# Performance work log

Measured on AMD Instinct MI355X. Metric: run time of the kernel, lower is better.

The kernel has to match this reference:

```python
import jax, jax.numpy as jnp
import numpy as np

F_DIM = 128
EC = 32
SYM = 16
B = 4
S = 2048
EPS = 1e-5


def rpy_to_rot(a):
    # roll-pitch-yaw euler angles [..., 3] -> rotation matrices [..., 3, 3]
    c, s = jnp.cos(a), jnp.sin(a)
    cr, cp, cy = c[..., 0], c[..., 1], c[..., 2]
    sr, sp, sy = s[..., 0], s[..., 1], s[..., 2]
    return jnp.stack([
        jnp.stack([cy * cp, cy * sp * sr - sy * cr, cy * sp * cr + sy * sr], -1),
        jnp.stack([sy * cp, sy * sp * sr + cy * cr, sy * sp * cr - cy * sr], -1),
        jnp.stack([-sp, cp * sr, cp * cr], -1),
    ], -2)


def _tile(x):
    # tile_for_symgroups: append the first SYM (symmetric) elements again
    return jnp.concatenate([x, x[:, :SYM]], axis=1)


def _cbn(emb, h, bw, bb, gw, gb):
    # BatchedCBatchNormLayer in eval mode: running_mean=0, running_var=1 buffers
    beta = emb @ bw + bb
    gamma = emb @ gw + gb
    hn = h * (1.0 / np.sqrt(1.0 + EPS))
    return gamma[:, None, :] * hn + beta[:, None, :]


def _forward(packed_vector, samples, fc1_w, fc1_b, bn1_beta_w, bn1_beta_b, bn1_gamma_w, bn1_gamma_b, rfc1_w, rfc1_b, bn2_beta_w, bn2_beta_b, bn2_gamma_w, bn2_gamma_b, rfc2_w, rfc2_b, bn3_beta_w, bn3_beta_b, bn3_gamma_w, bn3_gamma_b, fc2_w, fc2_b):
    b = packed_vector.shape[0]
    constants = packed_vector[..., 0:1]
    centers = packed_vector[..., 1:4]
    radii = packed_vector[..., 4:10]   # 3 stds + 3 euler angles
    iparams = packed_vector[..., 10:]

    eff_const = _tile(constants)       # [B, E, 1]
    eff_centers = _tile(centers)       # [B, E, 3]
    eff_radii = _tile(radii)           # [B, E, 6]
    eff_iparams = _tile(iparams)       # [B, E, F]
    e = EC + SYM

    samp = jnp.broadcast_to(samples[:, None], (b, EC, samples.shape[1], 3))
    sym_samp = samp[:, :SYM] * jnp.array([1.0, 1.0, -1.0], samples.dtype)  # left-right reflection
    eff_samples = jnp.concatenate([samp, sym_samp], axis=1)                # [B, E, S, 3]

    # quadric algebraic distance (quadric has only the constant term at [3, 3])
    quad = jnp.zeros((b, e, 4, 4), samples.dtype).at[..., 3, 3].set(eff_const[..., 0])
    diff = eff_samples - eff_centers[:, :, None, :]
    homog = jnp.concatenate([diff, jnp.ones(diff.shape[:-1] + (1,), diff.dtype)], -1)
    half = jnp.einsum('besj,beij->besi', homog, quad)
    per_element_constants = jnp.sum(half * homog, -1, keepdims=True)       # [B, E, S, 1]

    # gaussian RBF influence weights in the rotated element frame
    rot = rpy_to_rot(eff_radii[..., 3:6])                                  # [B, E, 3, 3]
    local_diff = jnp.einsum('besi,beij->besj', diff, rot)                  # R^T (x - c)
    std = jnp.maximum(eff_radii[..., :3], 1e-4)
    local_samples = local_diff / std[:, :, None, :]                        # world2local = S(1/std) R^T T(-c)
    per_element_weights = jnp.exp(-0.5 * jnp.sum(local_samples ** 2, -1, keepdims=True))

    # OccNet decoder over flattened batch*element
    emb = eff_iparams.reshape(b * e, F_DIM)
    x = local_samples.reshape(b * e, -1, 3)
    h = x @ fc1_w + fc1_b                                                  # [BE, S, F]
    h = _cbn(emb, h, bn1_beta_w, bn1_beta_b, bn1_gamma_w, bn1_gamma_b)
    init_h = h
    h = jax.nn.relu(h) @ rfc1_w + rfc1_b
    h = _cbn(emb, h, bn2_beta_w, bn2_beta_b, bn2_gamma_w, bn2_gamma_b)
    h = jax.nn.relu(h) @ rfc2_w + rfc2_b
    h = init_h + h
    h = _cbn(emb, h, bn3_beta_w, bn3_beta_b, bn3_gamma_w, bn3_gamma_b)
    vals = h @ fc2_w + fc2_b                                               # [BE, S, 1]

    implicit_values = vals.reshape(b, e, -1, 1)
    residuals = 1.0 + implicit_values
    local_decisions = per_element_constants * per_element_weights * residuals
    sdf = jnp.sum(local_decisions, axis=1)                                 # [B, S, 1]
    return sdf


def setup_inputs():
    key = jax.random.key(0)
    ks = jax.random.split(key, 16)
    const = jax.random.normal(ks[0], (B, EC, 1), dtype=jnp.float32) * 0.5
    centers = jax.random.normal(ks[1], (B, EC, 3), dtype=jnp.float32) * 0.5
    radii_std = jax.random.uniform(ks[2], (B, EC, 3), dtype=jnp.float32, minval=0.1, maxval=0.4)
    euler = jax.random.uniform(ks[3], (B, EC, 3), dtype=jnp.float32, minval=-np.pi, maxval=np.pi)
    iparams = jax.random.normal(ks[4], (B, EC, F_DIM), dtype=jnp.float32)
    packed_vector = jnp.concatenate([const, centers, radii_std, euler, iparams], -1)
    samples = jax.random.normal(ks[5], (B, S, 3), dtype=jnp.float32)

    def lin(k, i, o):
        kw, kb = jax.random.split(k)
        return (jax.random.normal(kw, (i, o), dtype=jnp.float32) / np.sqrt(i),
                jax.random.normal(kb, (o,), dtype=jnp.float32) * 0.01)

    fc1_w, fc1_b = lin(ks[6], 3, F_DIM)
    bn1_beta_w, bn1_beta_b = lin(ks[7], F_DIM, F_DIM)
    bn1_gamma_w, bn1_gamma_b = lin(ks[8], F_DIM, F_DIM)
    rfc1_w, rfc1_b = lin(ks[9], F_DIM, F_DIM)
    bn2_beta_w, bn2_beta_b = lin(ks[10], F_DIM, F_DIM)
    bn2_gamma_w, bn2_gamma_b = lin(ks[11], F_DIM, F_DIM)
    rfc2_w, rfc2_b = lin(ks[12], F_DIM, F_DIM)
    bn3_beta_w, bn3_beta_b = lin(ks[13], F_DIM, F_DIM)
    bn3_gamma_w, bn3_gamma_b = lin(ks[14], F_DIM, F_DIM)
    fc2_w, fc2_b = lin(ks[15], F_DIM, 1)
    return {"packed_vector": packed_vector, "samples": samples,
            "fc1_w": fc1_w, "fc1_b": fc1_b,
            "bn1_beta_w": bn1_beta_w, "bn1_beta_b": bn1_beta_b,
            "bn1_gamma_w": bn1_gamma_w, "bn1_gamma_b": bn1_gamma_b,
            "rfc1_w": rfc1_w, "rfc1_b": rfc1_b,
            "bn2_beta_w": bn2_beta_w, "bn2_beta_b": bn2_beta_b,
            "bn2_gamma_w": bn2_gamma_w, "bn2_gamma_b": bn2_gamma_b,
            "rfc2_w": rfc2_w, "rfc2_b": rfc2_b,
            "bn3_beta_w": bn3_beta_w, "bn3_beta_b": bn3_beta_b,
            "bn3_gamma_w": bn3_gamma_w, "bn3_gamma_b": bn3_gamma_b,
            "fc2_w": fc2_w, "fc2_b": fc2_b}


def reference(packed_vector, samples, fc1_w, fc1_b, bn1_beta_w, bn1_beta_b, bn1_gamma_w, bn1_gamma_b, rfc1_w, rfc1_b, bn2_beta_w, bn2_beta_b, bn2_gamma_w, bn2_gamma_b, rfc2_w, rfc2_b, bn3_beta_w, bn3_beta_b, bn3_gamma_w, bn3_gamma_b, fc2_w, fc2_b):
    return _forward(packed_vector, samples, fc1_w, fc1_b, bn1_beta_w, bn1_beta_b, bn1_gamma_w, bn1_gamma_b, rfc1_w, rfc1_b, bn2_beta_w, bn2_beta_b, bn2_gamma_w, bn2_gamma_b, rfc2_w, rfc2_b, bn3_beta_w, bn3_beta_b, bn3_gamma_w, bn3_gamma_b, fc2_w, fc2_b)
```

## Files before the change

### kernel.cpp

```cpp
#include <hip/hip_runtime.h>
#include <math.h>

#define B_   4
#define EC_  32
#define E_   48
#define S_   2048
#define F_   128

typedef __attribute__((ext_vector_type(8)))  short short8;
typedef __attribute__((ext_vector_type(4)))  float f32x4;
typedef __attribute__((ext_vector_type(16))) float f32x16;

__device__ __align__(16) short g_A1[4 * 8 * 64 * 8];

#define PKF2 1440
__device__ __align__(16) float g_bepark[B_ * E_ * PKF2];

static __device__ __forceinline__ short f2bf(float x) {
    unsigned u = __float_as_uint(x);
    unsigned r = (u + 0x7FFFu + ((u >> 16) & 1u)) >> 16;
    return (short)r;
}

__global__ __launch_bounds__(256) void precompute_kernel(
    const float* __restrict__ packed,
    const float* __restrict__ fc1w, const float* __restrict__ fc1b,
    const float* __restrict__ bw1, const float* __restrict__ bb1,
    const float* __restrict__ gw1, const float* __restrict__ gb1,
    const float* __restrict__ rb1g, const float* __restrict__ rw1,
    const float* __restrict__ bw2, const float* __restrict__ bb2,
    const float* __restrict__ gw2, const float* __restrict__ gb2,
    const float* __restrict__ rw2, const float* __restrict__ rb2g,
    const float* __restrict__ bw3, const float* __restrict__ bb3,
    const float* __restrict__ gw3, const float* __restrict__ gb3,
    const float* __restrict__ fc2w, const float* __restrict__ fc2b)
{
    const int be = blockIdx.x;

    if (be >= 192) {
        const int unit = (be - 192) * 4 + (threadIdx.x >> 6);
        const int l  = threadIdx.x & 63;
        const int MT = unit >> 3;
        const int ks = unit & 7;
        const int fo = MT * 32 + (l & 31);
        const int q1 = l >> 5;
        short8 v;
        #pragma unroll
        for (int j = 0; j < 8; ++j) {
            const int fi = (ks >> 1) * 32 + (ks & 1) * 16 + ((j >> 2) & 1) * 8 +
                           (j & 3) + q1 * 4;
            v[j] = f2bf(rw1[fi * F_ + fo]);
        }
        *(short8*)&g_A1[((MT * 8 + ks) * 64 + l) * 8] = v;
        return;
    }

    const int b  = be / E_;
    const int e  = be - b * E_;
    const int ec = (e < EC_) ? e : (e - EC_);
    const float* pv = packed + (size_t)(b * EC_ + ec) * 138;
    float* P = g_bepark + (size_t)be * PKF2;

    __shared__ float emb[F_];
    __shared__ float part[6][2][F_];
    __shared__ float g3s[F_];
    __shared__ float redbuf[F_];

    const int t = threadIdx.x & 127;
    const int h = threadIdx.x >> 7;
    if (h == 0) emb[t] = pv[10 + t];
    __syncthreads();

    float a0 = 0.f, a1 = 0.f, a2 = 0.f, a3 = 0.f, a4 = 0.f, a5 = 0.f;
    for (int k = h * 64; k < h * 64 + 64; ++k) {
        const float ek = emb[k];
        a0 = fmaf(ek, bw1[k * F_ + t], a0);
        a1 = fmaf(ek, gw1[k * F_ + t], a1);
        a2 = fmaf(ek, bw2[k * F_ + t], a2);
        a3 = fmaf(ek, gw2[k * F_ + t], a3);
        a4 = fmaf(ek, bw3[k * F_ + t], a4);
        a5 = fmaf(ek, gw3[k * F_ + t], a5);
    }
    part[0][h][t] = a0; part[1][h][t] = a1; part[2][h][t] = a2;
    part[3][h][t] = a3; part[4][h][t] = a4; part[5][h][t] = a5;
    __syncthreads();

    const float inv = 0.99999500003749984f;
    if (h == 0) {
        const float sb1 = part[0][0][t] + part[0][1][t];
        const float sg1 = part[1][0][t] + part[1][1][t];
        const float sb2 = part[2][0][t] + part[2][1][t];
        const float sg2 = part[3][0][t] + part[3][1][t];
        const float sb3 = part[4][0][t] + part[4][1][t];
        const float sg3 = part[5][0][t] + part[5][1][t];

        const float g1p = (sg1 + gb1[t]) * inv;
        const float b1  =  sb1 + bb1[t];
        const float g2p = (sg2 + gb2[t]) * inv;
        const float b2p = fmaf(g2p, rb1g[t], sb2 + bb2[t]);
        const float g3  = (sg3 + gb3[t]) * inv * fc2w[t];

        P[0 * F_ + t] = g2p;
        P[1 * F_ + t] = b2p;
        g3s[t] = g3;
        redbuf[t] = (sb3 + bb3[t]) * fc2w[t] + g3 * rb2g[t];

        const float w0p = g1p * fc1w[t];
        const float w1p = g1p * fc1w[F_ + t];
        const float w2p = g1p * fc1w[2 * F_ + t];
        const float pbp = fmaf(g1p, fc1b[t], b1);
        short* A0 = (short*)(P + 416);
        const int MTl = t >> 5, fl = t & 31;
        short8 v  = {f2bf(w0p), f2bf(w1p), f2bf(w2p), f2bf(pbp), 0, 0, 0, 0};
        short8 zz = {0, 0, 0, 0, 0, 0, 0, 0};
        *(short8*)&A0[(MTl * 64 + fl) * 8]      = v;
        *(short8*)&A0[(MTl * 64 + 32 + fl) * 8] = zz;

        part[1][0][t] = g3 * w0p;
        part[2][0][t] = g3 * w1p;
        part[3][0][t] = g3 * w2p;
        part[4][0][t] = g3 * pbp;
    }
    __syncthreads();

    {
        float ua = 0.f;
        const float* wrow = rw2 + (size_t)t * F_ + h * 64;
        #pragma unroll
        for (int f4 = 0; f4 < 64; f4 += 4) {
            const f32x4 wv = *(const f32x4*)&wrow[f4];
            const int fb = h * 64 + f4;
            ua = fmaf(wv[0], g3s[fb + 0], ua);
            ua = fmaf(wv[1], g3s[fb + 1], ua);
            ua = fmaf(wv[2], g3s[fb + 2], ua);
            ua = fmaf(wv[3], g3s[fb + 3], ua);
        }
        part[0][h][t] = ua;
    }
    __syncthreads();
    if (h == 0) P[2 * F_ + t] = part[0][0][t] + part[0][1][t];

    if (threadIdx.x == 0) {
        float cb = fc2b[0];
        float w30 = 0.f, w31 = 0.f, w32 = 0.f, w3b = 0.f;
        for (int i = 0; i < F_; ++i) {
            cb  += redbuf[i];
            w30 += part[1][0][i];
            w31 += part[2][0][i];
            w32 += part[3][0][i];
            w3b += part[4][0][i];
        }
        P[400] = w30; P[401] = w31; P[402] = w32; P[403] = w3b + cb;

        const float sx = fmaxf(pv[4], 1e-4f);
        const float sy = fmaxf(pv[5], 1e-4f);
        const float sz = fmaxf(pv[6], 1e-4f);
        const float ar = pv[7], ap = pv[8], ay = pv[9];
        const float cr = cosf(ar), sr = sinf(ar);
        const float cp = cosf(ap), sp = sinf(ap);
        const float cyw = cosf(ay), syw = sinf(ay);
        float* g = P + 384;
        g[0] = pv[0]; g[1] = pv[1]; g[2] = pv[2]; g[3] = pv[3];
        g[4] = 1.f / sx; g[5] = 1.f / sy; g[6] = 1.f / sz;
        g[7]  = cyw * cp;  g[8]  = cyw * sp * sr - syw * cr;  g[9]  = cyw * sp * cr + syw * sr;
        g[10] = syw * cp;  g[11] = syw * sp * sr + cyw * cr;  g[12] = syw * sp * cr - cyw * sr;
        g[13] = -sp;       g[14] = cp * sr;                   g[15] = cp * cr;
    }
}

__global__ __launch_bounds__(256, 2) void ldif_main(
    const float* __restrict__ samples, float* __restrict__ out)
{
    const int bid = blockIdx.x;
    const int eg  = bid & 7;
    const int seg = (bid >> 3) & 15;
    const int b   = bid >> 7;
    const int be0 = b * E_ + eg * 6;

    __shared__ __align__(16) short lsA1[4 * 8 * 64 * 8];
    __shared__ __align__(16) float lsPar[6 * 416];

    const int tid = threadIdx.x;

    {
        const f32x4* src = (const f32x4*)g_A1;
        f32x4* dst = (f32x4*)lsA1;
        #pragma unroll
        for (int i = 0; i < 8; ++i) dst[i * 256 + tid] = src[i * 256 + tid];
    }
    for (int i = tid; i < 624; i += 256) {
        const int ei = i / 104;
        const int o4 = i - ei * 104;
        ((f32x4*)lsPar)[ei * 104 + o4] =
            *(const f32x4*)&g_bepark[(size_t)(be0 + ei) * PKF2 + o4 * 4];
    }
    __syncthreads();

    const int l   = tid & 63;
    const int w   = tid >> 6;
    const int q1  = l >> 5;
    const int l31 = l & 31;
    const int sidx = seg * 128 + w * 32 + l31;
    const f32x16 z16 = {0.f,0.f,0.f,0.f,0.f,0.f,0.f,0.f,
                        0.f,0.f,0.f,0.f,0.f,0.f,0.f,0.f};

    const float* sp = samples + ((size_t)b * S_ + sidx) * 3;
    const float xs = sp[0], ys = sp[1], zs0 = sp[2];

    float acc = 0.f;

    #pragma unroll
    for (int ee = 0; ee < 6; ++ee) {
        const int pe = ee * 416;
        const float* gg = &lsPar[pe + 384];
        const float* w3 = &lsPar[pe + 400];
        const int e = eg * 6 + ee;

        float cwgt, sval;
        union { short8 s8; unsigned u[4]; } b0u;
        b0u.u[0] = 0; b0u.u[1] = 0; b0u.u[2] = 0; b0u.u[3] = 0;
        {
            const float zz = (e >= EC_) ? -zs0 : zs0;
            const float dx = xs - gg[1], dy = ys - gg[2], dz = zz - gg[3];
            const float l0 = (dx * gg[7] + dy * gg[10] + dz * gg[13]) * gg[4];
            const float l1 = (dx * gg[8] + dy * gg[11] + dz * gg[14]) * gg[5];
            const float l2 = (dx * gg[9] + dy * gg[12] + dz * gg[15]) * gg[6];
            cwgt = gg[0] * __expf(-0.5f * (l0 * l0 + l1 * l1 + l2 * l2));
            sval = fmaf(l0, w3[0], fmaf(l1, w3[1], fmaf(l2, w3[2], w3[3])));
            if (q1 == 0) {
                const float one = 1.0f;
                unsigned p01, p23;
                asm("v_cvt_pk_bf16_f32 %0, %1, %2" : "=v"(p01) : "v"(l0), "v"(l1));
                asm("v_cvt_pk_bf16_f32 %0, %1, %2" : "=v"(p23) : "v"(l2), "v"(one));
                b0u.u[0] = p01; b0u.u[1] = p23;
            }
        }
        const short8 b0 = b0u.s8;

        const short* A0g = (const short*)(g_bepark + (size_t)(be0 + ee) * PKF2 + 416);
        f32x16 d0[4];
        #pragma unroll
        for (int MT = 0; MT < 4; ++MT) {
            const short8 a0 = *(const short8*)&A0g[(MT * 64 + l) * 8];
            d0[MT] = __builtin_amdgcn_mfma_f32_32x32x16_bf16(a0, b0, z16, 0, 0, 0);
        }

        f32x16 d1[4];
        #pragma unroll
        for (int MT = 0; MT < 4; ++MT) d1[MT] = z16;
        #pragma unroll
        for (int ks = 0; ks < 8; ++ks) {
            union { short8 s8; unsigned u[4]; } b1u;
            #pragma unroll
            for (int jj = 0; jj < 4; ++jj) {
                const int j0 = jj * 2;
                const int r0 = (j0 & 3) + 4 * ((j0 >> 2) & 1) + 8 * (ks & 1);
                const float v0 = fmaxf(d0[ks >> 1][r0], 0.f);
                const float v1 = fmaxf(d0[ks >> 1][r0 + 1], 0.f);
                asm("v_cvt_pk_bf16_f32 %0, %1, %2" : "=v"(b1u.u[jj]) : "v"(v0), "v"(v1));
            }
            const short8 b1 = b1u.s8;
            #pragma unroll
            for (int MT = 0; MT < 4; ++MT) {
                const short8 a = *(const short8*)&lsA1[((MT * 8 + ks) * 64 + l) * 8];
                d1[MT] = __builtin_amdgcn_mfma_f32_32x32x16_bf16(a, b1, d1[MT], 0, 0, 0);
            }
        }

        float part = 0.f;
        #pragma unroll
        for (int MT = 0; MT < 4; ++MT) {
            #pragma unroll
            for (int c = 0; c < 4; ++c) {
                const int fb = MT * 32 + c * 8 + q1 * 4;
                const f32x4 g2 = *(const f32x4*)&lsPar[pe + fb];
                const f32x4 b2 = *(const f32x4*)&lsPar[pe + 128 + fb];
                const f32x4 uu = *(const f32x4*)&lsPar[pe + 256 + fb];
                #pragma unroll
                for (int i = 0; i < 4; ++i) {
                    const float tt = fmaf(g2[i], d1[MT][c * 4 + i], b2[i]);
                    part = fmaf(fmaxf(tt, 0.f), uu[i], part);
                }
            }
        }
        part += __shfl_xor(part, 32);
        acc = fmaf(cwgt, 1.f + part + sval, acc);
    }

    if (l < 32) atomicAdd(&out[(size_t)b * S_ + sidx], acc);
}

extern "C" void kernel_launch(void* const* d_in, const int* in_sizes, int n_in,
                              void* d_out, int out_size, void* d_ws, size_t ws_size,
                              hipStream_t stream) {
    (void)in_sizes; (void)n_in; (void)d_ws; (void)ws_size;

    const float* packed  = (const float*)d_in[0];
    const float* samples = (const float*)d_in[1];
    const float* fc1w = (const float*)d_in[2];
    const float* fc1b = (const float*)d_in[3];
    const float* bw1  = (const float*)d_in[4];
    const float* bb1  = (const float*)d_in[5];
    const float* gw1  = (const float*)d_in[6];
    const float* gb1  = (const float*)d_in[7];
    const float* rw1  = (const float*)d_in[8];
    const float* rb1  = (const float*)d_in[9];
    const float* bw2  = (const float*)d_in[10];
    const float* bb2  = (const float*)d_in[11];
    const float* gw2  = (const float*)d_in[12];
    const float* gb2  = (const float*)d_in[13];
    const float* rw2  = (const float*)d_in[14];
    const float* rb2  = (const float*)d_in[15];
    const float* bw3  = (const float*)d_in[16];
    const float* bb3  = (const float*)d_in[17];
    const float* gw3  = (const float*)d_in[18];
    const float* gb3  = (const float*)d_in[19];
    const float* fc2w = (const float*)d_in[20];
    const float* fc2b = (const float*)d_in[21];
    float* out = (float*)d_out;

    (void)hipMemsetAsync(out, 0, (size_t)out_size * sizeof(float), stream);

    precompute_kernel<<<200, 256, 0, stream>>>(
        packed, fc1w, fc1b,
        bw1, bb1, gw1, gb1, rb1, rw1,
        bw2, bb2, gw2, gb2, rw2, rb2,
        bw3, bb3, gw3, gb3, fc2w, fc2b);

    ldif_main<<<512, 256, 0, stream>>>(samples, out);
}
```

Before: 39.30 us.

## Replace memset and atomics with workspace partials plus reduce kernel; widen precompute blocks

The main kernel now writes per-element-group partial sums into a workspace instead of atomically adding into a zeroed output. A small reduce kernel sums the 8 partials, which removes both the memset launch and the atomic contention. The precompute kernel also moves to 512 threads per block, splitting its K loops four ways to shorten each thread's serial dot products. The cost is an extra kernel launch and workspace traffic in place of the memset launch.

```diff
diff --git a/kernel.cpp b/kernel.cpp
--- a/kernel.cpp
+++ b/kernel.cpp
@@ -22,7 +22,7 @@
     return (short)r;
 }
 
-__global__ __launch_bounds__(256) void precompute_kernel(
+__global__ __launch_bounds__(512) void precompute_kernel(
     const float* __restrict__ packed,
     const float* __restrict__ fc1w, const float* __restrict__ fc1b,
     const float* __restrict__ bw1, const float* __restrict__ bb1,
@@ -38,7 +38,7 @@
     const int be = blockIdx.x;
 
     if (be >= 192) {
-        const int unit = (be - 192) * 4 + (threadIdx.x >> 6);
+        const int unit = (be - 192) * 8 + (threadIdx.x >> 6);
         const int l  = threadIdx.x & 63;
         const int MT = unit >> 3;
         const int ks = unit & 7;
@@ -62,7 +62,7 @@
     float* P = g_bepark + (size_t)be * PKF2;
 
     __shared__ float emb[F_];
-    __shared__ float part[6][2][F_];
+    __shared__ float part[6][4][F_];
     __shared__ float g3s[F_];
     __shared__ float redbuf[F_];
 
@@ -72,7 +72,7 @@
     __syncthreads();
 
     float a0 = 0.f, a1 = 0.f, a2 = 0.f, a3 = 0.f, a4 = 0.f, a5 = 0.f;
-    for (int k = h * 64; k < h * 64 + 64; ++k) {
+    for (int k = h * 32; k < h * 32 + 32; ++k) {
         const float ek = emb[k];
         a0 = fmaf(ek, bw1[k * F_ + t], a0);
         a1 = fmaf(ek, gw1[k * F_ + t], a1);
@@ -87,12 +87,12 @@
 
     const float inv = 0.99999500003749984f;
     if (h == 0) {
-        const float sb1 = part[0][0][t] + part[0][1][t];
-        const float sg1 = part[1][0][t] + part[1][1][t];
-        const float sb2 = part[2][0][t] + part[2][1][t];
-        const float sg2 = part[3][0][t] + part[3][1][t];
-        const float sb3 = part[4][0][t] + part[4][1][t];
-        const float sg3 = part[5][0][t] + part[5][1][t];
+        const float sb1 = part[0][0][t] + part[0][1][t] + part[0][2][t] + part[0][3][t];
+        const float sg1 = part[1][0][t] + part[1][1][t] + part[1][2][t] + part[1][3][t];
+        const float sb2 = part[2][0][t] + part[2][1][t] + part[2][2][t] + part[2][3][t];
+        const float sg2 = part[3][0][t] + part[3][1][t] + part[3][2][t] + part[3][3][t];
+        const float sb3 = part[4][0][t] + part[4][1][t] + part[4][2][t] + part[4][3][t];
+        const float sg3 = part[5][0][t] + part[5][1][t] + part[5][2][t] + part[5][3][t];
 
         const float g1p = (sg1 + gb1[t]) * inv;
         const float b1  =  sb1 + bb1[t];
@@ -125,20 +125,21 @@
 
     {
         float ua = 0.f;
-        const float* wrow = rw2 + (size_t)t * F_ + h * 64;
-        #pragma unroll
-        for (int f4 = 0; f4 < 64; f4 += 4) {
+        const float* wrow = rw2 + (size_t)t * F_ + h * 32;
+        #pragma unroll
+        for (int f4 = 0; f4 < 32; f4 += 4) {
             const f32x4 wv = *(const f32x4*)&wrow[f4];
-            const int fb = h * 64 + f4;
+            const int fb = h * 32 + f4;
             ua = fmaf(wv[0], g3s[fb + 0], ua);
             ua = fmaf(wv[1], g3s[fb + 1], ua);
             ua = fmaf(wv[2], g3s[fb + 2], ua);
             ua = fmaf(wv[3], g3s[fb + 3], ua);
         }
-        part[0][h][t] = ua;
-    }
-    __syncthreads();
-    if (h == 0) P[2 * F_ + t] = part[0][0][t] + part[0][1][t];
+        part[5][h][t] = ua;
+    }
+    __syncthreads();
+    if (h == 0)
+        P[2 * F_ + t] = part[5][0][t] + part[5][1][t] + part[5][2][t] + part[5][3][t];
 
     if (threadIdx.x == 0) {
         float cb = fc2b[0];
@@ -169,7 +170,7 @@
 }
 
 __global__ __launch_bounds__(256, 2) void ldif_main(
-    const float* __restrict__ samples, float* __restrict__ out)
+    const float* __restrict__ samples, float* __restrict__ ws)
 {
     const int bid = blockIdx.x;
     const int eg  = bid & 7;
@@ -287,13 +288,25 @@
         acc = fmaf(cwgt, 1.f + part + sval, acc);
     }
 
-    if (l < 32) atomicAdd(&out[(size_t)b * S_ + sidx], acc);
+    if (l < 32)
+        ws[(size_t)eg * (B_ * S_) + (size_t)b * S_ + sidx] = acc;
+}
+
+__global__ __launch_bounds__(256) void reduce_kernel(
+    const float* __restrict__ ws, float* __restrict__ out)
+{
+    const int i = blockIdx.x * 256 + threadIdx.x;
+    float s = 0.f;
+    #pragma unroll
+    for (int eg = 0; eg < 8; ++eg)
+        s += ws[(size_t)eg * (B_ * S_) + i];
+    out[i] = s;
 }
 
 extern "C" void kernel_launch(void* const* d_in, const int* in_sizes, int n_in,
                               void* d_out, int out_size, void* d_ws, size_t ws_size,
                               hipStream_t stream) {
-    (void)in_sizes; (void)n_in; (void)d_ws; (void)ws_size;
+    (void)in_sizes; (void)n_in; (void)out_size; (void)ws_size;
 
     const float* packed  = (const float*)d_in[0];
     const float* samples = (const float*)d_in[1];
@@ -318,14 +331,15 @@
     const float* fc2w = (const float*)d_in[20];
     const float* fc2b = (const float*)d_in[21];
     float* out = (float*)d_out;
-
-    (void)hipMemsetAsync(out, 0, (size_t)out_size * sizeof(float), stream);
-
-    precompute_kernel<<<200, 256, 0, stream>>>(
+    float* ws  = (float*)d_ws;
+
+    precompute_kernel<<<196, 512, 0, stream>>>(
         packed, fc1w, fc1b,
         bw1, bb1, gw1, gb1, rb1, rw1,
         bw2, bb2, gw2, gb2, rw2, rb2,
         bw3, bb3, gw3, gb3, fc2w, fc2b);
 
-    ldif_main<<<512, 256, 0, stream>>>(samples, out);
-}
+    ldif_main<<<512, 256, 0, stream>>>(samples, ws);
+
+    reduce_kernel<<<32, 256, 0, stream>>>(ws, out);
+}
```

New measurement: 35.17 us. 10.5% less time.
